# Optimization experiments

Measured on AMD Instinct MI355X. Metric: run time of the kernel, lower is better.

## Reference

```python
import jax, jax.numpy as jnp
import numpy as np

N, E, D, H = 50000, 600000, 128, 128
SLOPE = 0.01  # default negative_slope of F.leaky_relu / nn.LeakyReLU


def leaky(x):
    return jnp.where(x >= 0, x, SLOPE * x)


def gcn_conv(x, src, dst, W, b, n):
    """PyG GCNConv: x' = D^{-1/2}(A+I)D^{-1/2} (x W) + b, symmetric norm with self-loops."""
    h = x @ W  # [n, out]
    ones = jnp.ones(src.shape[0], h.dtype)
    deg = jax.ops.segment_sum(ones, dst, num_segments=n) + 1.0  # +1 for self-loop
    dinv = jax.lax.rsqrt(deg)  # deg >= 1 always
    norm = dinv[src] * dinv[dst]  # per-edge coefficient
    msg = h[src] * norm[:, None]  # gather + scale: [E, out]
    agg = jax.ops.segment_sum(msg, dst, num_segments=n)  # scatter-add
    agg = agg + h * (dinv * dinv)[:, None]  # self-loop term
    return agg + b


def setup_inputs() -> dict:
    key = jax.random.key(0)
    ks = jax.random.split(key, 16)
    kaiming = lambda k, fi, fo: jax.random.normal(k, (fi, fo), jnp.float32) * np.sqrt(2.0 / fi)
    return {
        "x": jax.random.normal(ks[0], (N, D), jnp.float32),
        "edge_index": jax.random.randint(ks[1], (2, E), 0, N, jnp.int64 if jax.config.jax_enable_x64 else jnp.int32),
        "gen_data": jax.random.normal(ks[2], (N, H), jnp.float32),
        "Wc1": kaiming(ks[3], D, H), "bc1": jnp.zeros((H,), jnp.float32),
        "Wc2": kaiming(ks[4], H, H), "bc2": jnp.zeros((H,), jnp.float32),
        "Wm1": kaiming(ks[5], H, H), "bm1": jnp.zeros((H,), jnp.float32),
        "Wm2": kaiming(ks[6], H, H), "bm2": jnp.zeros((H,), jnp.float32),
        "Wp1": kaiming(ks[7], H, H), "bp1": jnp.zeros((H,), jnp.float32),
        "Wp2": kaiming(ks[8], H, H), "bp2": jnp.zeros((H,), jnp.float32),
    }


def reference(x, edge_index, gen_data, Wc1, bc1, Wc2, bc2, Wm1, bm1, Wm2, bm2, Wp1, bp1, Wp2, bp2):
    src, dst = edge_index[0], edge_index[1]
    lambd = 0.5
    # GraphEncoder4Link
    h = leaky(gcn_conv(x, src, dst, Wc1, bc1, N))
    h = leaky(gcn_conv(h, src, dst, Wc2, bc2, N) + h)
    h = leaky((leaky(h @ Wm1 + bm1) @ Wm2 + bm2) + h)
    # lambd interpolation with gen_data
    out = lambd * h + (1.0 - lambd) * gen_data
    # proj MLP
    out = leaky(leaky(out @ Wp1 + bp1) @ Wp2 + bp2)
    return out
```

## Files before the change

### kernel.cpp

```cpp
#include <hip/hip_runtime.h>
#include <cstdint>
#include <cstddef>

#define HH 128
#define SLOPE 0.01f

typedef __attribute__((ext_vector_type(8))) __bf16 bf16x8;
typedef __attribute__((ext_vector_type(4))) float f32x4;

__device__ __forceinline__ float lrelu(float x) { return x >= 0.f ? x : SLOPE * x; }
__device__ __forceinline__ unsigned short f2b(float f) {
  union { float f; unsigned u; } v; v.f = f;
  unsigned r = v.u + 0x7fffu + ((v.u >> 16) & 1u);
  return (unsigned short)(r >> 16);
}
__device__ __forceinline__ float b2f(unsigned short u) {
  union { unsigned u; float f; } v; v.u = ((unsigned)u) << 16; return v.f;
}

__device__ __forceinline__ int lofs(int r, int k) {
  return (r << 7) + ((((k >> 3) ^ r) & 15) << 3) + (k & 7);
}


__global__ __launch_bounds__(256) void count_kernel(const int* __restrict__ dst,
                                                    int* __restrict__ cnt, int nE) {
  int e = blockIdx.x * 256 + threadIdx.x;
  if (e < nE) atomicAdd(&cnt[dst[e]], 1);
}

__global__ __launch_bounds__(1024) void scan1_kernel(int* __restrict__ cnt,
                                                     int* __restrict__ rowptr,
                                                     int* __restrict__ bsum,
                                                     float* __restrict__ dinv, int n) {
  __shared__ int wsum[16];
  const int tid = threadIdx.x;
  const int lane = tid & 63, wid = tid >> 6;
  int i = blockIdx.x * 1024 + tid;
  int v = (i < n) ? cnt[i] : 0;
  int x = v;
#pragma unroll
  for (int off = 1; off < 64; off <<= 1) {
    int y = __shfl_up(x, off, 64);
    if (lane >= off) x += y;
  }
  if (lane == 63) wsum[wid] = x;
  __syncthreads();
  if (tid == 0) {
    int s = 0;
#pragma unroll
    for (int w = 0; w < 16; ++w) { int t = wsum[w]; wsum[w] = s; s += t; }
    bsum[blockIdx.x] = s;
  }
  __syncthreads();
  if (i < n) {
    rowptr[i] = wsum[wid] + x - v;
    dinv[i] = rsqrtf((float)v + 1.0f);
    cnt[i] = 0;
  }
}

__global__ __launch_bounds__(64) void scan2_kernel(int* __restrict__ bsum, int nb,
                                                   int* __restrict__ rowptr, int n, int E) {
  int lane = threadIdx.x;
  int v = (lane < nb) ? bsum[lane] : 0;
  int x = v;
#pragma unroll
  for (int off = 1; off < 64; off <<= 1) {
    int y = __shfl_up(x, off, 64);
    if (lane >= off) x += y;
  }
  if (lane < nb) bsum[lane] = x - v;
  if (lane == 0) rowptr[n] = E;
}

__global__ __launch_bounds__(1024) void scan3_kernel(int* __restrict__ rowptr,
                                                     const int* __restrict__ bsum, int n) {
  int i = blockIdx.x * 1024 + threadIdx.x;
  if (i < n) rowptr[i] += bsum[blockIdx.x];
}

__global__ __launch_bounds__(256) void fill_kernel(const int* __restrict__ src,
                                                   const int* __restrict__ dst,
                                                   const int* __restrict__ rowptr,
                                                   int* __restrict__ cursor,
                                                   const float* __restrict__ dinv,
                                                   int2* __restrict__ csr, int nE) {
  int e = blockIdx.x * 256 + threadIdx.x;
  if (e >= nE) return;
  int d = dst[e], s = src[e];
  int pos = rowptr[d] + atomicAdd(&cursor[d], 1);
  int2 ent;
  ent.x = s;
  ent.y = __float_as_int(dinv[s] * dinv[d]);
  csr[pos] = ent;
}

__global__ __launch_bounds__(256) void pack_kernel(const float* W0, const float* W1,
                                                   const float* W2, const float* W3,
                                                   const float* W4, const float* W5,
                                                   unsigned short* __restrict__ out) {
  const float* Ws[6] = {W0, W1, W2, W3, W4, W5};
  const float* W = Ws[blockIdx.y];
  int f = blockIdx.x * 256 + threadIdx.x;
  int j = f & 7, L = (f >> 3) & 63, c = (f >> 9) & 7, t = f >> 12;
  int k = t * 32 + (L >> 4) * 8 + j;
  int n = c * 16 + (L & 15);
  out[(size_t)blockIdx.y * 16384 + f] = f2b(W[k * HH + n]);
}


__device__ __forceinline__ void mfma_stage(const unsigned short* __restrict__ Alds,
                                           const bf16x8* __restrict__ Wf,
                                           int arow, int lane, int quad, f32x4* acc) {
#pragma unroll
  for (int c = 0; c < 8; ++c) acc[c] = (f32x4){0.f, 0.f, 0.f, 0.f};
#pragma unroll
  for (int t = 0; t < 4; ++t) {
    bf16x8 a = *(const bf16x8*)&Alds[lofs(arow, t * 32 + quad * 8)];
#pragma unroll
    for (int c = 0; c < 8; ++c)
      acc[c] = __builtin_amdgcn_mfma_f32_16x16x32_bf16(a, Wf[(t * 8 + c) * 64 + lane], acc[c], 0, 0, 0);
  }
}


__global__ __launch_bounds__(256) void gemm_conv(const float* __restrict__ A,
                                                 const unsigned short* __restrict__ Wp,
                                                 unsigned short* __restrict__ out, int nrows) {
  __shared__ __align__(16) unsigned short Al[64 * HH];
  const int tid = threadIdx.x;
  const int row0 = blockIdx.x * 64;

  for (int i = tid; i < 2048; i += 256) {
    int r = i >> 5, c = (i & 31) << 2;
    int gr = row0 + r;
    float4 v = make_float4(0.f, 0.f, 0.f, 0.f);
    if (gr < nrows) v = *(const float4*)(A + (size_t)gr * HH + c);
    ushort4 o;
    o.x = f2b(v.x); o.y = f2b(v.y); o.z = f2b(v.z); o.w = f2b(v.w);
    *(ushort4*)&Al[lofs(r, c)] = o;
  }
  __syncthreads();

  const int lane = tid & 63, wave = tid >> 6;
  const int m = lane & 15, quad = lane >> 4;
  const int arow = wave * 16 + m;

  f32x4 acc[8];
  mfma_stage(Al, (const bf16x8*)Wp, arow, lane, quad, acc);

#pragma unroll
  for (int c = 0; c < 8; ++c) {
    int col = c * 16 + m;
#pragma unroll
    for (int g = 0; g < 4; ++g) {
      int row = row0 + wave * 16 + quad * 4 + g;
      if (row < nrows) out[(size_t)row * HH + col] = f2b(acc[c][g]);
    }
  }
}


template <int RES, int OUTBF>
__global__ __launch_bounds__(256) void agg_kernel(const unsigned short* __restrict__ h,
                                                  const int* __restrict__ rowptr,
                                                  const int2* __restrict__ csr,
                                                  const float* __restrict__ dinv,
                                                  const float* __restrict__ bias,
                                                  const float* __restrict__ res,
                                                  void* __restrict__ outv, int n) {
  int node = blockIdx.x * 4 + (threadIdx.x >> 6);
  if (node >= n) return;
  int lane = threadIdx.x & 63;
  int c = lane << 1;
  int j = rowptr[node], end = rowptr[node + 1];
  float ax = 0.f, ay = 0.f;
  for (; j + 8 <= end; j += 8) {
    int2 e[8];
    ushort2 r[8];
#pragma unroll
    for (int q = 0; q < 8; ++q) e[q] = csr[j + q];
#pragma unroll
    for (int q = 0; q < 8; ++q) r[q] = *(const ushort2*)(h + (size_t)e[q].x * HH + c);
#pragma unroll
    for (int q = 0; q < 8; ++q) {
      float nv = __int_as_float(e[q].y);
      ax = fmaf(b2f(r[q].x), nv, ax); ay = fmaf(b2f(r[q].y), nv, ay);
    }
  }
  for (; j + 2 <= end; j += 2) {
    int2 e0 = csr[j], e1 = csr[j + 1];
    ushort2 r0 = *(const ushort2*)(h + (size_t)e0.x * HH + c);
    ushort2 r1 = *(const ushort2*)(h + (size_t)e1.x * HH + c);
    float n0 = __int_as_float(e0.y), n1 = __int_as_float(e1.y);
    ax = fmaf(b2f(r0.x), n0, ax); ay = fmaf(b2f(r0.y), n0, ay);
    ax = fmaf(b2f(r1.x), n1, ax); ay = fmaf(b2f(r1.y), n1, ay);
  }
  if (j < end) {
    int2 e0 = csr[j];
    float n0 = __int_as_float(e0.y);
    ushort2 r0 = *(const ushort2*)(h + (size_t)e0.x * HH + c);
    ax = fmaf(b2f(r0.x), n0, ax); ay = fmaf(b2f(r0.y), n0, ay);
  }
  float di = dinv[node], d2 = di * di;
  ushort2 hs = *(const ushort2*)(h + (size_t)node * HH + c);
  float2 b = *(const float2*)(bias + c);
  float ox = ax + b2f(hs.x) * d2 + b.x;
  float oy = ay + b2f(hs.y) * d2 + b.y;
  if (RES) {
    float2 r = *(const float2*)(res + (size_t)node * HH + c);
    ox += r.x; oy += r.y;
  }
  ox = lrelu(ox); oy = lrelu(oy);
  if (OUTBF) {
    ushort2 o; o.x = f2b(ox); o.y = f2b(oy);
    *(ushort2*)((unsigned short*)outv + (size_t)node * HH + c) = o;
  } else {
    *(float2*)((float*)outv + (size_t)node * HH + c) = make_float2(ox, oy);
  }
}


__global__ __launch_bounds__(256) void fusedMLP(const unsigned short* __restrict__ f2bf,
                                                const unsigned short* __restrict__ Wm1p,
                                                const unsigned short* __restrict__ Wm2p,
                                                const unsigned short* __restrict__ Wp1p,
                                                const unsigned short* __restrict__ Wp2p,
                                                const float* __restrict__ bm1,
                                                const float* __restrict__ bm2,
                                                const float* __restrict__ bp1,
                                                const float* __restrict__ bp2,
                                                const float* __restrict__ gen,
                                                float* __restrict__ out, int n) {
  __shared__ __align__(16) unsigned short Al[64 * HH];
  __shared__ __align__(16) unsigned short Bl[64 * HH];
  __shared__ __align__(16) unsigned short Cl[64 * HH];
  const int tid = threadIdx.x;
  const int row0 = blockIdx.x * 64;

  for (int i = tid; i < 1024; i += 256) {
    int r = i >> 4, k = (i & 15) << 3;
    int gr = row0 + r;
    float4 v = make_float4(0.f, 0.f, 0.f, 0.f);
    if (gr < n) v = *(const float4*)(f2bf + (size_t)gr * HH + k);
    *(float4*)&Al[lofs(r, k)] = v;
  }
  for (int i = tid; i < 2048; i += 256) {
    int r = i >> 5, c = (i & 31) << 2;
    int gr = row0 + r;
    float4 v = make_float4(0.f, 0.f, 0.f, 0.f);
    if (gr < n) v = *(const float4*)(gen + (size_t)gr * HH + c);
    ushort4 o;
    o.x = f2b(v.x); o.y = f2b(v.y); o.z = f2b(v.z); o.w = f2b(v.w);
    *(ushort4*)&Cl[lofs(r, c)] = o;
  }
  __syncthreads();

  const int lane = tid & 63, wave = tid >> 6;
  const int m = lane & 15, quad = lane >> 4;
  const int arow = wave * 16 + m;
  f32x4 acc[8];

  mfma_stage(Al, (const bf16x8*)Wm1p, arow, lane, quad, acc);
#pragma unroll
  for (int cc = 0; cc < 8; ++cc) {
    int col = cc * 16 + m;
    float b1 = bm1[col];
#pragma unroll
    for (int g = 0; g < 4; ++g) {
      int lrow = wave * 16 + quad * 4 + g;
      Bl[lofs(lrow, col)] = f2b(lrelu(acc[cc][g] + b1));
    }
  }
  __syncthreads();

  mfma_stage(Bl, (const bf16x8*)Wm2p, arow, lane, quad, acc);
#pragma unroll
  for (int cc = 0; cc < 8; ++cc) {
    int col = cc * 16 + m;
    float b2 = bm2[col];
#pragma unroll
    for (int g = 0; g < 4; ++g) {
      int lrow = wave * 16 + quad * 4 + g;
      float f2v = b2f(Al[lofs(lrow, col)]);
      float gv = b2f(Cl[lofs(lrow, col)]);
      float v = lrelu(acc[cc][g] + b2 + f2v);
      Al[lofs(lrow, col)] = f2b(0.5f * (v + gv));
    }
  }
  __syncthreads();

  mfma_stage(Al, (const bf16x8*)Wp1p, arow, lane, quad, acc);
#pragma unroll
  for (int cc = 0; cc < 8; ++cc) {
    int col = cc * 16 + m;
    float b3 = bp1[col];
#pragma unroll
    for (int g = 0; g < 4; ++g) {
      int lrow = wave * 16 + quad * 4 + g;
      Bl[lofs(lrow, col)] = f2b(lrelu(acc[cc][g] + b3));
    }
  }
  __syncthreads();

  mfma_stage(Bl, (const bf16x8*)Wp2p, arow, lane, quad, acc);
#pragma unroll
  for (int cc = 0; cc < 8; ++cc) {
    int col = cc * 16 + m;
    float b4 = bp2[col];
#pragma unroll
    for (int g = 0; g < 4; ++g) {
      int row = row0 + wave * 16 + quad * 4 + g;
      if (row < n) out[(size_t)row * HH + col] = lrelu(acc[cc][g] + b4);
    }
  }
}


extern "C" void kernel_launch(void* const* d_in, const int* in_sizes, int n_in,
                              void* d_out, int out_size, void* d_ws, size_t ws_size,
                              hipStream_t stream) {
  const float* x   = (const float*)d_in[0];
  const int* ei    = (const int*)d_in[1];
  const float* gen = (const float*)d_in[2];
  const float* Wc1 = (const float*)d_in[3];
  const float* bc1 = (const float*)d_in[4];
  const float* Wc2 = (const float*)d_in[5];
  const float* bc2 = (const float*)d_in[6];
  const float* Wm1 = (const float*)d_in[7];
  const float* bm1 = (const float*)d_in[8];
  const float* Wm2 = (const float*)d_in[9];
  const float* bm2 = (const float*)d_in[10];
  const float* Wp1 = (const float*)d_in[11];
  const float* bp1 = (const float*)d_in[12];
  const float* Wp2 = (const float*)d_in[13];
  const float* bp2 = (const float*)d_in[14];

  const int N = in_sizes[0] / HH;
  const int E = in_sizes[1] / 2;
  const int* src = ei;
  const int* dst = ei + E;

  char* ws = (char*)d_ws;
  size_t off = 0;
  auto alloc = [&](size_t bytes) { void* p = ws + off; off += (bytes + 255) & ~(size_t)255; return p; };
  float* dinv            = (float*)alloc((size_t)N * 4);
  int*   rowptr          = (int*)  alloc((size_t)(N + 1) * 4);
  int*   cursor          = (int*)  alloc((size_t)N * 4);
  int*   bsum            = (int*)  alloc((size_t)64 * 4);
  int2*  csr             = (int2*) alloc((size_t)E * 8);
  unsigned short* h_bf   = (unsigned short*)alloc((size_t)N * HH * 2);
  unsigned short* t2_bf  = (unsigned short*)alloc((size_t)N * HH * 2);
  unsigned short* f2_bf  = (unsigned short*)alloc((size_t)N * HH * 2);
  float* f1_f32          = (float*)alloc((size_t)N * HH * 4);
  unsigned short* packed = (unsigned short*)alloc((size_t)6 * 16384 * 2);
  float* fOut = (float*)d_out;

  const int gblocks = (N + 63) / 64;
  const int eblocks = (E + 255) / 256;
  const int ablocks = (N + 3) / 4;
  const int sblocks = (N + 1023) / 1024;

  pack_kernel<<<dim3(64, 6), 256, 0, stream>>>(Wc1, Wc2, Wm1, Wm2, Wp1, Wp2, packed);

  hipMemsetAsync(cursor, 0, (size_t)N * 4, stream);
  count_kernel<<<eblocks, 256, 0, stream>>>(dst, cursor, E);
  scan1_kernel<<<sblocks, 1024, 0, stream>>>(cursor, rowptr, bsum, dinv, N);
  scan2_kernel<<<1, 64, 0, stream>>>(bsum, sblocks, rowptr, N, E);
  scan3_kernel<<<sblocks, 1024, 0, stream>>>(rowptr, bsum, N);
  fill_kernel<<<eblocks, 256, 0, stream>>>(src, dst, rowptr, cursor, dinv, csr, E);

  gemm_conv<<<gblocks, 256, 0, stream>>>(x, packed + 0 * 16384, h_bf, N);
  agg_kernel<0, 0><<<ablocks, 256, 0, stream>>>(h_bf, rowptr, csr, dinv, bc1, nullptr, f1_f32, N);
  gemm_conv<<<gblocks, 256, 0, stream>>>(f1_f32, packed + 1 * 16384, t2_bf, N);
  agg_kernel<1, 1><<<ablocks, 256, 0, stream>>>(t2_bf, rowptr, csr, dinv, bc2, f1_f32, f2_bf, N);
  fusedMLP<<<gblocks, 256, 0, stream>>>(f2_bf,
                                        packed + 2 * 16384, packed + 3 * 16384,
                                        packed + 4 * 16384, packed + 5 * 16384,
                                        bm1, bm2, bp1, bp2, gen, fOut, N);
}
```

Before: 307.7 us.

## Use single-wave blocks for GEMM and fused MLP kernels, dropping block barriers

The conv GEMM and the fused MLP now run as one 64-thread wave per 16-row tile instead of 256-thread blocks over 64 rows. The GEMM loads A rows straight into MFMA fragments in registers, with no LDS staging and no barrier. The MLP keeps small per-wave LDS tiles, swaps __syncthreads for an lgkmcnt wait, holds gen values in registers instead of an LDS tile, and hoists the bias loads. The aim is to remove block barriers and LDS traffic and to raise occupancy. The cost is four times as many blocks, each re-reading the packed weights, and the correctness of the MLP now rests on the wave-level LDS wait alone.

```diff
diff --git a/kernel.cpp b/kernel.cpp
--- a/kernel.cpp
+++ b/kernel.cpp
@@ -6,6 +6,7 @@
 #define SLOPE 0.01f
 
 typedef __attribute__((ext_vector_type(8))) __bf16 bf16x8;
+typedef __attribute__((ext_vector_type(8))) unsigned short ushort8v;
 typedef __attribute__((ext_vector_type(4))) float f32x4;
 
 __device__ __forceinline__ float lrelu(float x) { return x >= 0.f ? x : SLOPE * x; }
@@ -21,6 +22,8 @@
 __device__ __forceinline__ int lofs(int r, int k) {
   return (r << 7) + ((((k >> 3) ^ r) & 15) << 3) + (k & 7);
 }
+
+#define WAVE_SYNC() asm volatile("s_waitcnt lgkmcnt(0)" ::: "memory")
 
 
 __global__ __launch_bounds__(256) void count_kernel(const int* __restrict__ dst,
@@ -125,37 +128,47 @@
 }
 
 
-__global__ __launch_bounds__(256) void gemm_conv(const float* __restrict__ A,
-                                                 const unsigned short* __restrict__ Wp,
-                                                 unsigned short* __restrict__ out, int nrows) {
-  __shared__ __align__(16) unsigned short Al[64 * HH];
-  const int tid = threadIdx.x;
-  const int row0 = blockIdx.x * 64;
-
-  for (int i = tid; i < 2048; i += 256) {
-    int r = i >> 5, c = (i & 31) << 2;
-    int gr = row0 + r;
-    float4 v = make_float4(0.f, 0.f, 0.f, 0.f);
-    if (gr < nrows) v = *(const float4*)(A + (size_t)gr * HH + c);
-    ushort4 o;
-    o.x = f2b(v.x); o.y = f2b(v.y); o.z = f2b(v.z); o.w = f2b(v.w);
-    *(ushort4*)&Al[lofs(r, c)] = o;
-  }
-  __syncthreads();
-
-  const int lane = tid & 63, wave = tid >> 6;
+__global__ __launch_bounds__(64) void gemm_conv(const float* __restrict__ A,
+                                                const unsigned short* __restrict__ Wp,
+                                                unsigned short* __restrict__ out, int nrows) {
+  const int lane = threadIdx.x;
+  const int row0 = blockIdx.x * 16;
   const int m = lane & 15, quad = lane >> 4;
-  const int arow = wave * 16 + m;
+  const int gr = row0 + m;
+  const bool rok = gr < nrows;
+  const float* Arow = A + (size_t)gr * HH;
+  const bf16x8* Wf = (const bf16x8*)Wp;
+
+  bf16x8 af[4];
+#pragma unroll
+  for (int t = 0; t < 4; ++t) {
+    const int k = t * 32 + quad * 8;
+    float4 lo = make_float4(0.f, 0.f, 0.f, 0.f), hi = lo;
+    if (rok) {
+      lo = *(const float4*)(Arow + k);
+      hi = *(const float4*)(Arow + k + 4);
+    }
+    union { ushort8v u; bf16x8 b; } cv;
+    cv.u[0] = f2b(lo.x); cv.u[1] = f2b(lo.y); cv.u[2] = f2b(lo.z); cv.u[3] = f2b(lo.w);
+    cv.u[4] = f2b(hi.x); cv.u[5] = f2b(hi.y); cv.u[6] = f2b(hi.z); cv.u[7] = f2b(hi.w);
+    af[t] = cv.b;
+  }
 
   f32x4 acc[8];
-  mfma_stage(Al, (const bf16x8*)Wp, arow, lane, quad, acc);
+#pragma unroll
+  for (int c = 0; c < 8; ++c) acc[c] = (f32x4){0.f, 0.f, 0.f, 0.f};
+#pragma unroll
+  for (int t = 0; t < 4; ++t)
+#pragma unroll
+    for (int c = 0; c < 8; ++c)
+      acc[c] = __builtin_amdgcn_mfma_f32_16x16x32_bf16(af[t], Wf[(t * 8 + c) * 64 + lane], acc[c], 0, 0, 0);
 
 #pragma unroll
   for (int c = 0; c < 8; ++c) {
     int col = c * 16 + m;
 #pragma unroll
     for (int g = 0; g < 4; ++g) {
-      int row = row0 + wave * 16 + quad * 4 + g;
+      int row = row0 + quad * 4 + g;
       if (row < nrows) out[(size_t)row * HH + col] = f2b(acc[c][g]);
     }
   }
@@ -222,97 +235,103 @@
 }
 
 
-__global__ __launch_bounds__(256) void fusedMLP(const unsigned short* __restrict__ f2bf,
-                                                const unsigned short* __restrict__ Wm1p,
-                                                const unsigned short* __restrict__ Wm2p,
-                                                const unsigned short* __restrict__ Wp1p,
-                                                const unsigned short* __restrict__ Wp2p,
-                                                const float* __restrict__ bm1,
-                                                const float* __restrict__ bm2,
-                                                const float* __restrict__ bp1,
-                                                const float* __restrict__ bp2,
-                                                const float* __restrict__ gen,
-                                                float* __restrict__ out, int n) {
-  __shared__ __align__(16) unsigned short Al[64 * HH];
-  __shared__ __align__(16) unsigned short Bl[64 * HH];
-  __shared__ __align__(16) unsigned short Cl[64 * HH];
-  const int tid = threadIdx.x;
-  const int row0 = blockIdx.x * 64;
-
-  for (int i = tid; i < 1024; i += 256) {
-    int r = i >> 4, k = (i & 15) << 3;
+__global__ __launch_bounds__(64) void fusedMLP(const unsigned short* __restrict__ f2bf,
+                                               const unsigned short* __restrict__ Wm1p,
+                                               const unsigned short* __restrict__ Wm2p,
+                                               const unsigned short* __restrict__ Wp1p,
+                                               const unsigned short* __restrict__ Wp2p,
+                                               const float* __restrict__ bm1,
+                                               const float* __restrict__ bm2,
+                                               const float* __restrict__ bp1,
+                                               const float* __restrict__ bp2,
+                                               const float* __restrict__ gen,
+                                               float* __restrict__ out, int n) {
+  __shared__ __align__(16) unsigned short Al[16 * HH];
+  __shared__ __align__(16) unsigned short Bl[16 * HH];
+  const int lane = threadIdx.x;
+  const int row0 = blockIdx.x * 16;
+  const int m = lane & 15, quad = lane >> 4;
+
+#pragma unroll
+  for (int i = 0; i < 4; ++i) {
+    int idx = i * 64 + lane;
+    int r = idx >> 4, k = (idx & 15) << 3;
     int gr = row0 + r;
-    float4 v = make_float4(0.f, 0.f, 0.f, 0.f);
-    if (gr < n) v = *(const float4*)(f2bf + (size_t)gr * HH + k);
-    *(float4*)&Al[lofs(r, k)] = v;
-  }
-  for (int i = tid; i < 2048; i += 256) {
-    int r = i >> 5, c = (i & 31) << 2;
-    int gr = row0 + r;
-    float4 v = make_float4(0.f, 0.f, 0.f, 0.f);
-    if (gr < n) v = *(const float4*)(gen + (size_t)gr * HH + c);
-    ushort4 o;
-    o.x = f2b(v.x); o.y = f2b(v.y); o.z = f2b(v.z); o.w = f2b(v.w);
-    *(ushort4*)&Cl[lofs(r, c)] = o;
-  }
-  __syncthreads();
-
-  const int lane = tid & 63, wave = tid >> 6;
-  const int m = lane & 15, quad = lane >> 4;
-  const int arow = wave * 16 + m;
+    ushort8v v = {0, 0, 0, 0, 0, 0, 0, 0};
+    if (gr < n) v = *(const ushort8v*)(f2bf + (size_t)gr * HH + k);
+    *(ushort8v*)&Al[lofs(r, k)] = v;
+  }
+
+  float genv[8][4];
+#pragma unroll
+  for (int cc = 0; cc < 8; ++cc)
+#pragma unroll
+    for (int g = 0; g < 4; ++g) {
+      int grow = row0 + quad * 4 + g;
+      genv[cc][g] = (grow < n) ? gen[(size_t)grow * HH + cc * 16 + m] : 0.f;
+    }
+
   f32x4 acc[8];
-
-  mfma_stage(Al, (const bf16x8*)Wm1p, arow, lane, quad, acc);
+  WAVE_SYNC();
+
+  float b1v[8];
+#pragma unroll
+  for (int cc = 0; cc < 8; ++cc) b1v[cc] = bm1[cc * 16 + m];
+  mfma_stage(Al, (const bf16x8*)Wm1p, m, lane, quad, acc);
 #pragma unroll
   for (int cc = 0; cc < 8; ++cc) {
     int col = cc * 16 + m;
-    float b1 = bm1[col];
-#pragma unroll
-    for (int g = 0; g < 4; ++g) {
-      int lrow = wave * 16 + quad * 4 + g;
-      Bl[lofs(lrow, col)] = f2b(lrelu(acc[cc][g] + b1));
-    }
-  }
-  __syncthreads();
-
-  mfma_stage(Bl, (const bf16x8*)Wm2p, arow, lane, quad, acc);
+#pragma unroll
+    for (int g = 0; g < 4; ++g) {
+      int lrow = quad * 4 + g;
+      Bl[lofs(lrow, col)] = f2b(lrelu(acc[cc][g] + b1v[cc]));
+    }
+  }
+  WAVE_SYNC();
+
+  float b2v[8];
+#pragma unroll
+  for (int cc = 0; cc < 8; ++cc) b2v[cc] = bm2[cc * 16 + m];
+  mfma_stage(Bl, (const bf16x8*)Wm2p, m, lane, quad, acc);
 #pragma unroll
   for (int cc = 0; cc < 8; ++cc) {
     int col = cc * 16 + m;
-    float b2 = bm2[col];
-#pragma unroll
-    for (int g = 0; g < 4; ++g) {
-      int lrow = wave * 16 + quad * 4 + g;
+#pragma unroll
+    for (int g = 0; g < 4; ++g) {
+      int lrow = quad * 4 + g;
       float f2v = b2f(Al[lofs(lrow, col)]);
-      float gv = b2f(Cl[lofs(lrow, col)]);
-      float v = lrelu(acc[cc][g] + b2 + f2v);
-      Al[lofs(lrow, col)] = f2b(0.5f * (v + gv));
-    }
-  }
-  __syncthreads();
-
-  mfma_stage(Al, (const bf16x8*)Wp1p, arow, lane, quad, acc);
+      float v = lrelu(acc[cc][g] + b2v[cc] + f2v);
+      Al[lofs(lrow, col)] = f2b(0.5f * (v + genv[cc][g]));
+    }
+  }
+  WAVE_SYNC();
+
+  float b3v[8];
+#pragma unroll
+  for (int cc = 0; cc < 8; ++cc) b3v[cc] = bp1[cc * 16 + m];
+  mfma_stage(Al, (const bf16x8*)Wp1p, m, lane, quad, acc);
 #pragma unroll
   for (int cc = 0; cc < 8; ++cc) {
     int col = cc * 16 + m;
-    float b3 = bp1[col];
-#pragma unroll
-    for (int g = 0; g < 4; ++g) {
-      int lrow = wave * 16 + quad * 4 + g;
-      Bl[lofs(lrow, col)] = f2b(lrelu(acc[cc][g] + b3));
-    }
-  }
-  __syncthreads();
-
-  mfma_stage(Bl, (const bf16x8*)Wp2p, arow, lane, quad, acc);
+#pragma unroll
+    for (int g = 0; g < 4; ++g) {
+      int lrow = quad * 4 + g;
+      Bl[lofs(lrow, col)] = f2b(lrelu(acc[cc][g] + b3v[cc]));
+    }
+  }
+  WAVE_SYNC();
+
+  float b4v[8];
+#pragma unroll
+  for (int cc = 0; cc < 8; ++cc) b4v[cc] = bp2[cc * 16 + m];
+  mfma_stage(Bl, (const bf16x8*)Wp2p, m, lane, quad, acc);
 #pragma unroll
   for (int cc = 0; cc < 8; ++cc) {
     int col = cc * 16 + m;
-    float b4 = bp2[col];
-#pragma unroll
-    for (int g = 0; g < 4; ++g) {
-      int row = row0 + wave * 16 + quad * 4 + g;
-      if (row < n) out[(size_t)row * HH + col] = lrelu(acc[cc][g] + b4);
+#pragma unroll
+    for (int g = 0; g < 4; ++g) {
+      int row = row0 + quad * 4 + g;
+      if (row < n) out[(size_t)row * HH + col] = lrelu(acc[cc][g] + b4v[cc]);
     }
   }
 }
@@ -357,7 +376,7 @@
   unsigned short* packed = (unsigned short*)alloc((size_t)6 * 16384 * 2);
   float* fOut = (float*)d_out;
 
-  const int gblocks = (N + 63) / 64;
+  const int wblocks = (N + 15) / 16;
   const int eblocks = (E + 255) / 256;
   const int ablocks = (N + 3) / 4;
   const int sblocks = (N + 1023) / 1024;
@@ -371,12 +390,12 @@
   scan3_kernel<<<sblocks, 1024, 0, stream>>>(rowptr, bsum, N);
   fill_kernel<<<eblocks, 256, 0, stream>>>(src, dst, rowptr, cursor, dinv, csr, E);
 
-  gemm_conv<<<gblocks, 256, 0, stream>>>(x, packed + 0 * 16384, h_bf, N);
+  gemm_conv<<<wblocks, 64, 0, stream>>>(x, packed + 0 * 16384, h_bf, N);
   agg_kernel<0, 0><<<ablocks, 256, 0, stream>>>(h_bf, rowptr, csr, dinv, bc1, nullptr, f1_f32, N);
-  gemm_conv<<<gblocks, 256, 0, stream>>>(f1_f32, packed + 1 * 16384, t2_bf, N);
+  gemm_conv<<<wblocks, 64, 0, stream>>>(f1_f32, packed + 1 * 16384, t2_bf, N);
   agg_kernel<1, 1><<<ablocks, 256, 0, stream>>>(t2_bf, rowptr, csr, dinv, bc2, f1_f32, f2_bf, N);
-  fusedMLP<<<gblocks, 256, 0, stream>>>(f2_bf,
-                                        packed + 2 * 16384, packed + 3 * 16384,
-                                        packed + 4 * 16384, packed + 5 * 16384,
-                                        bm1, bm2, bp1, bp2, gen, fOut, N);
-}
+  fusedMLP<<<wblocks, 64, 0, stream>>>(f2_bf,
+                                       packed + 2 * 16384, packed + 3 * 16384,
+                                       packed + 4 * 16384, packed + 5 * 16384,
+                                       bm1, bm2, bp1, bp2, gen, fOut, N);
+}
```

New measurement: 301.0 us. -2.2%, faster.
